# Kernel tuning notes

Hardware: AMD Instinct MI355X
Metric: run time of the kernel (lower is better)

Reference implementation:

```python
import jax, jax.numpy as jnp
import numpy as np

B, S, D = 2, 1024, 1024
N_HEADS = 16
R = 128
M = 8
N_NEURONS = 256


def group_gate(gate, n_basis):
    # gate: [B,S,N] -> [B,S,M], sum over consecutive groups, then normalize
    b, s, n = gate.shape
    gs = n // n_basis  # exact by construction (256/8)
    g = gate.reshape(b, s, n_basis, gs).sum(axis=-1)
    return g / (g.sum(axis=-1, keepdims=True) + 1e-8)


def feature_fn(x, neurons, weights):
    # x:[B,S,D], neurons:[M,D,R], weights:[B,S,M] -> h:[B,S,R]
    all_h = jnp.einsum('bsd,mdr->bsmr', x, neurons)
    return jnp.einsum('bsmr,bsm->bsr', all_h, weights)


def restore_fn(h, neurons, weights):
    # h:[B,S,R], neurons:[M,R,D], weights:[B,S,M] -> [B,S,D]
    pre = jnp.einsum('bsr,bsm->bsmr', h, weights)
    return jnp.einsum('bsmr,mrd->bsd', pre, neurons)


def setup_inputs() -> dict:
    key = jax.random.key(0)
    ks = jax.random.split(key, 9)
    sc = 0.02
    return {
        'x': jax.random.normal(ks[0], (B, S, D), jnp.float32),
        'qk_f': jax.random.normal(ks[1], (M, D, R), jnp.float32) * sc,
        'qk_r': jax.random.normal(ks[2], (M, R, D), jnp.float32) * sc,
        'v_f': jax.random.normal(ks[3], (M, D, R), jnp.float32) * sc,
        'v_r': jax.random.normal(ks[4], (M, R, D), jnp.float32) * sc,
        'Wg_q': jax.random.normal(ks[5], (D, N_NEURONS), jnp.float32) * sc,
        'Wg_k': jax.random.normal(ks[6], (D, N_NEURONS), jnp.float32) * sc,
        'Wg_v': jax.random.normal(ks[7], (D, N_NEURONS), jnp.float32) * sc,
        'W_O': jax.random.normal(ks[8], (D, D), jnp.float32) * sc,
    }


def reference(x, qk_f, qk_r, v_f, v_r, Wg_q, Wg_k, Wg_v, W_O):
    # Router gates (softmax over neuron dim), then grouped per basis
    g_Q = jax.nn.softmax(jnp.einsum('bsd,dn->bsn', x, Wg_q), axis=-1)
    g_K = jax.nn.softmax(jnp.einsum('bsd,dn->bsn', x, Wg_k), axis=-1)
    g_V = jax.nn.softmax(jnp.einsum('bsd,dn->bsn', x, Wg_v), axis=-1)
    gQ_b = group_gate(g_Q, M)
    gK_b = group_gate(g_K, M)
    gV_b = group_gate(g_V, M)

    Q = restore_fn(feature_fn(x, qk_f, gQ_b), qk_r, gQ_b)
    K = restore_fn(feature_fn(x, qk_f, gK_b), qk_r, gK_b)
    V = restore_fn(feature_fn(x, v_f, gV_b), v_r, gV_b)

    d_head = D // N_HEADS
    Q = Q.reshape(B, S, N_HEADS, d_head).transpose(0, 2, 1, 3)
    K = K.reshape(B, S, N_HEADS, d_head).transpose(0, 2, 1, 3)
    V = V.reshape(B, S, N_HEADS, d_head).transpose(0, 2, 1, 3)

    scale = jnp.sqrt(jnp.float32(d_head))
    scores = jnp.einsum('bhsd,bhtd->bhst', Q, K) / scale
    causal = jnp.tril(jnp.ones((S, S), dtype=jnp.bool_))
    scores = jnp.where(causal, scores, jnp.finfo(scores.dtype).min)
    attn_w = jax.nn.softmax(scores, axis=-1)
    out = jnp.einsum('bhst,bhtd->bhsd', attn_w, V)
    out = out.transpose(0, 2, 1, 3).reshape(B, S, D)
    out = jnp.einsum('bsd,de->bse', out, W_O)
    return out
```

## Files before the change

### kernel.cpp

```cpp
#include <hip/hip_runtime.h>
#include <hip/hip_bf16.h>

#define BB 2
#define SS 1024
#define DD 1024
#define NH 16
#define DH 64
#define MM 8
#define RR 128
#define NN 256
#define NT (BB*SS)

using bf16 = __hip_bfloat16;

typedef __attribute__((ext_vector_type(8))) short short8;
typedef __attribute__((ext_vector_type(4))) short short4v;
typedef __attribute__((ext_vector_type(4))) float f32x4;

__device__ __forceinline__ void stf(float* p, size_t i, float v) { p[i] = v; }
__device__ __forceinline__ void stf(bf16* p, size_t i, float v) { p[i] = __float2bfloat16(v); }

#define GLD16(g, l) __builtin_amdgcn_global_load_lds( \
    (const __attribute__((address_space(1))) void*)(g), \
    (__attribute__((address_space(3))) void*)(l), 16, 0, 0)

__device__ __forceinline__ short8 lds_load8(const short* p) {
    short4v a = *(const short4v*)p;
    short4v b = *(const short4v*)(p + 4);
    short8 r;
    r[0] = a[0]; r[1] = a[1]; r[2] = a[2]; r[3] = a[3];
    r[4] = b[0]; r[5] = b[1]; r[6] = b[2]; r[7] = b[3];
    return r;
}

struct GemmZ {
    const bf16* A[5];
    const bf16* Bt[5];
    void* C[5];
    int N[5];
};

template <typename TC, int TAG>
__global__ __launch_bounds__(256) void mfma_gemm_64z(GemmZ P, int Kdim) {
    const int z = blockIdx.z;
    const int Nz = P.N[z];
    const int n0 = blockIdx.x * 128;
    if (n0 >= Nz) return;
    const bf16* __restrict__ A  = P.A[z];
    const bf16* __restrict__ Bt = P.Bt[z];
    TC* __restrict__ C = (TC*)P.C[z];

    const int tid = threadIdx.x;
    const int wave = tid >> 6, lane = tid & 63;
    const int quad = lane >> 4, l15 = lane & 15;
    const int wr = wave >> 1, wc = wave & 1;
    const int m0 = blockIdx.y * 64;

    __shared__ bf16 As[64 * 64];
    __shared__ bf16 Bs[128 * 64];

    f32x4 acc[2][4];
#pragma unroll
    for (int i = 0; i < 2; ++i)
#pragma unroll
        for (int j = 0; j < 4; ++j) acc[i][j] = (f32x4)0.f;

    for (int k0 = 0; k0 < Kdim; k0 += 64) {
        __syncthreads();
#pragma unroll
        for (int i = 0; i < 2; ++i) {
            const int L = i * 256 + wave * 64 + lane;
            const int row = L >> 3;
            const int gch = (L & 7) ^ ((row >> 1) & 7);
            GLD16(A + (size_t)(m0 + row) * Kdim + k0 + gch * 8, &As[(i * 256 + wave * 64) * 8]);
        }
#pragma unroll
        for (int i = 0; i < 4; ++i) {
            const int L = i * 256 + wave * 64 + lane;
            const int row = L >> 3;
            const int gch = (L & 7) ^ ((row >> 1) & 7);
            GLD16(Bt + (size_t)(n0 + row) * Kdim + k0 + gch * 8, &Bs[(i * 256 + wave * 64) * 8]);
        }
        __syncthreads();

#pragma unroll
        for (int kk = 0; kk < 2; ++kk) {
            short8 aF[2], bF[4];
#pragma unroll
            for (int bi = 0; bi < 2; ++bi) {
                int m = wr * 32 + bi * 16 + l15;
                int slot = (kk * 4 + quad) ^ ((m >> 1) & 7);
                aF[bi] = *(const short8*)&As[(m * 8 + slot) * 8];
            }
#pragma unroll
            for (int bj = 0; bj < 4; ++bj) {
                int n = wc * 64 + bj * 16 + l15;
                int slot = (kk * 4 + quad) ^ ((n >> 1) & 7);
                bF[bj] = *(const short8*)&Bs[(n * 8 + slot) * 8];
            }
#pragma unroll
            for (int bi = 0; bi < 2; ++bi)
#pragma unroll
                for (int bj = 0; bj < 4; ++bj)
                    acc[bi][bj] = __builtin_amdgcn_mfma_f32_16x16x32_bf16(aF[bi], bF[bj], acc[bi][bj], 0, 0, 0);
        }
    }

#pragma unroll
    for (int bi = 0; bi < 2; ++bi)
#pragma unroll
        for (int bj = 0; bj < 4; ++bj)
#pragma unroll
            for (int r = 0; r < 4; ++r) {
                int row = m0 + wr * 32 + bi * 16 + quad * 4 + r;
                int col = n0 + wc * 64 + bj * 16 + l15;
                stf(C, (size_t)row * Nz + col, acc[bi][bj][r]);
            }
}

template <typename TC>
__global__ __launch_bounds__(256) void mfma_gemm_64(
    const bf16* __restrict__ A, const bf16* __restrict__ Bt, TC* __restrict__ C,
    int Kdim, int Ndim) {
    const int tid = threadIdx.x;
    const int wave = tid >> 6, lane = tid & 63;
    const int quad = lane >> 4, l15 = lane & 15;
    const int wr = wave >> 1, wc = wave & 1;
    const int m0 = blockIdx.y * 64;
    const int n0 = blockIdx.x * 128;

    __shared__ bf16 As[64 * 64];
    __shared__ bf16 Bs[128 * 64];

    f32x4 acc[2][4];
#pragma unroll
    for (int i = 0; i < 2; ++i)
#pragma unroll
        for (int j = 0; j < 4; ++j) acc[i][j] = (f32x4)0.f;

    for (int k0 = 0; k0 < Kdim; k0 += 64) {
        __syncthreads();
#pragma unroll
        for (int i = 0; i < 2; ++i) {
            const int L = i * 256 + wave * 64 + lane;
            const int row = L >> 3;
            const int gch = (L & 7) ^ ((row >> 1) & 7);
            GLD16(A + (size_t)(m0 + row) * Kdim + k0 + gch * 8, &As[(i * 256 + wave * 64) * 8]);
        }
#pragma unroll
        for (int i = 0; i < 4; ++i) {
            const int L = i * 256 + wave * 64 + lane;
            const int row = L >> 3;
            const int gch = (L & 7) ^ ((row >> 1) & 7);
            GLD16(Bt + (size_t)(n0 + row) * Kdim + k0 + gch * 8, &Bs[(i * 256 + wave * 64) * 8]);
        }
        __syncthreads();

#pragma unroll
        for (int kk = 0; kk < 2; ++kk) {
            short8 aF[2], bF[4];
#pragma unroll
            for (int bi = 0; bi < 2; ++bi) {
                int m = wr * 32 + bi * 16 + l15;
                int slot = (kk * 4 + quad) ^ ((m >> 1) & 7);
                aF[bi] = *(const short8*)&As[(m * 8 + slot) * 8];
            }
#pragma unroll
            for (int bj = 0; bj < 4; ++bj) {
                int n = wc * 64 + bj * 16 + l15;
                int slot = (kk * 4 + quad) ^ ((n >> 1) & 7);
                bF[bj] = *(const short8*)&Bs[(n * 8 + slot) * 8];
            }
#pragma unroll
            for (int bi = 0; bi < 2; ++bi)
#pragma unroll
                for (int bj = 0; bj < 4; ++bj)
                    acc[bi][bj] = __builtin_amdgcn_mfma_f32_16x16x32_bf16(aF[bi], bF[bj], acc[bi][bj], 0, 0, 0);
        }
    }

#pragma unroll
    for (int bi = 0; bi < 2; ++bi)
#pragma unroll
        for (int bj = 0; bj < 4; ++bj)
#pragma unroll
            for (int r = 0; r < 4; ++r) {
                int row = m0 + wr * 32 + bi * 16 + quad * 4 + r;
                int col = n0 + wc * 64 + bj * 16 + l15;
                stf(C, (size_t)row * Ndim + col, acc[bi][bj][r]);
            }
}

struct ConvJobs {
    const float* src[9];
    bf16* dst[9];
    int K[9], R[9], G[9];
    int tEnd[9];
};

__global__ void convert_kernel(ConvJobs J) {
    __shared__ float tile[32][33];
    const int b = blockIdx.x;
    int j = 0;
    while (j < 8 && b >= J.tEnd[j]) ++j;
    const int local = b - (j > 0 ? J.tEnd[j - 1] : 0);
    const float* src = J.src[j];
    bf16* dst = J.dst[j];
    const int tid = threadIdx.x;

    if (J.G[j] == 0) {
        size_t base = (size_t)local * 4096 + (size_t)tid * 16;
        const float4* s4 = (const float4*)(src + base);
        short* d = (short*)(dst + base);
#pragma unroll
        for (int c = 0; c < 4; ++c) {
            float4 v = s4[c];
            short4v o;
            bf16 t0 = __float2bfloat16(v.x); o[0] = *(short*)&t0;
            bf16 t1 = __float2bfloat16(v.y); o[1] = *(short*)&t1;
            bf16 t2 = __float2bfloat16(v.z); o[2] = *(short*)&t2;
            bf16 t3 = __float2bfloat16(v.w); o[3] = *(short*)&t3;
            *(short4v*)(d + c * 4) = o;
        }
    } else {
        const int Kj = J.K[j], Rj = J.R[j];
        const int Rb = Rj >> 5, Kb = Kj >> 5;
        const int perG = Kb * Rb;
        const int g = local / perG;
        const int rem = local - g * perG;
        const int kb = rem / Rb, rb = rem - kb * Rb;
        const int tx = tid & 31, ty0 = tid >> 5;
        const float* s = src + ((size_t)(g * Kj + kb * 32) * Rj) + rb * 32 + tx;
#pragma unroll
        for (int p = 0; p < 4; ++p)
            tile[ty0 + p * 8][tx] = s[(size_t)(ty0 + p * 8) * Rj];
        __syncthreads();
        bf16* dd = dst + ((size_t)(g * Rj + rb * 32) * Kj) + kb * 32 + tx;
#pragma unroll
        for (int p = 0; p < 4; ++p)
            dd[(size_t)(ty0 + p * 8) * Kj] = __float2bfloat16(tile[tx][ty0 + p * 8]);
    }
}

__global__ void gate_combine(const bf16* __restrict__ logitsAll,
                             const bf16* __restrict__ allh,
                             bf16* __restrict__ preQ, bf16* __restrict__ preK,
                             bf16* __restrict__ preV) {
    const int t = blockIdx.x;
    const int n = threadIdx.x;
    const int wave = n >> 6, lane = n & 63;
    __shared__ float wred[3][4];
    __shared__ float sred[3][4];
    __shared__ float gred[3][8];

    float v[3], e[3];
#pragma unroll
    for (int z = 0; z < 3; ++z)
        v[z] = __bfloat162float(logitsAll[(size_t)z * NT * NN + (size_t)t * NN + n]);

    float mz[3];
#pragma unroll
    for (int z = 0; z < 3; ++z) {
        mz[z] = v[z];
#pragma unroll
        for (int off = 1; off <= 32; off <<= 1)
            mz[z] = fmaxf(mz[z], __shfl_xor(mz[z], off));
    }
    if (lane == 0) {
#pragma unroll
        for (int z = 0; z < 3; ++z) wred[z][wave] = mz[z];
    }
    __syncthreads();
    float gmax[3];
#pragma unroll
    for (int z = 0; z < 3; ++z)
        gmax[z] = fmaxf(fmaxf(wred[z][0], wred[z][1]), fmaxf(wred[z][2], wred[z][3]));

    float ws[3];
#pragma unroll
    for (int z = 0; z < 3; ++z) {
        e[z] = __expf(v[z] - gmax[z]);
        ws[z] = e[z];
#pragma unroll
        for (int off = 1; off <= 32; off <<= 1)
            ws[z] += __shfl_xor(ws[z], off);
    }
    if (lane == 0) {
#pragma unroll
        for (int z = 0; z < 3; ++z) sred[z][wave] = ws[z];
    }
    float gs[3];
#pragma unroll
    for (int z = 0; z < 3; ++z) {
        gs[z] = e[z];
#pragma unroll
        for (int off = 1; off <= 16; off <<= 1)
            gs[z] += __shfl_xor(gs[z], off);
    }
    __syncthreads();
    float total[3];
#pragma unroll
    for (int z = 0; z < 3; ++z)
        total[z] = sred[z][0] + sred[z][1] + sred[z][2] + sred[z][3];
    if ((n & 31) == 0) {
#pragma unroll
        for (int z = 0; z < 3; ++z) gred[z][n >> 5] = gs[z] / total[z];
    }
    __syncthreads();

    float gv[3][8];
#pragma unroll
    for (int z = 0; z < 3; ++z) {
        float tot = 0.f;
#pragma unroll
        for (int m = 0; m < 8; ++m) tot += gred[z][m];
        float inv = 1.0f / (tot + 1e-8f);
#pragma unroll
        for (int m = 0; m < 8; ++m) gv[z][m] = gred[z][m] * inv;
    }

    const int r0 = n & 127;
    const int half = n >> 7;
    const bf16* src_qk = allh + (size_t)t * 1024;
    const bf16* src_v  = allh + (size_t)NT * DD + (size_t)t * 1024;
    float hq = 0.f, hk = 0.f, hv = 0.f;
#pragma unroll
    for (int m = 0; m < 8; ++m) {
        float aqk = __bfloat162float(src_qk[m * 128 + r0]);
        float av  = __bfloat162float(src_v[m * 128 + r0]);
        hq += aqk * gv[0][m];
        hk += aqk * gv[1][m];
        hv += av  * gv[2][m];
    }
    __syncthreads();
#pragma unroll
    for (int mm = 0; mm < 4; ++mm) {
        int m = half * 4 + mm;
        size_t o = (size_t)t * 1024 + m * 128 + r0;
        preQ[o] = __float2bfloat16(hq * gv[0][m]);
        preK[o] = __float2bfloat16(hk * gv[1][m]);
        preV[o] = __float2bfloat16(hv * gv[2][m]);
    }
}

#define LDK 68

__global__ __launch_bounds__(256) void flash_attn_split(
    const bf16* __restrict__ Q, const bf16* __restrict__ K,
    const bf16* __restrict__ V, float* __restrict__ Opart,
    float* __restrict__ ml) {
    const int bx = blockIdx.x;
    const int c = bx & 511;
    const int second = bx >> 9;
    const int qt = second ? (c >> 5) : (15 - (c >> 5));
    const int half = second;
    const int bh = c & 31;
    const int b = bh >> 4;
    const int h = bh & 15;
    const int h0 = (qt + 2) >> 1;
    const int kt_lo = half ? h0 : 0;
    const int kt_hi = half ? (qt + 1) : h0;

    const int tid = threadIdx.x;
    const int wave = tid >> 6;
    const int lane = tid & 63;
    const int quad = lane >> 4;
    const int l15 = lane & 15;

    __shared__ short Ks[64 * LDK];
    __shared__ short Vt[64 * LDK];
    __shared__ short Ps[4 * 16 * LDK];

    const int q_row = qt * 64 + wave * 16 + l15;
    const bf16* qptr = Q + (size_t)(b * SS + q_row) * DD + h * DH + quad * 8;
    short8 aq0 = *(const short8*)qptr;
    short8 aq1 = *(const short8*)(qptr + 32);

    float m_r[4], l_r[4];
    f32x4 o[4];
#pragma unroll
    for (int r = 0; r < 4; ++r) { m_r[r] = -3.0e38f; l_r[r] = 0.f; }
#pragma unroll
    for (int cc = 0; cc < 4; ++cc) o[cc] = (f32x4)0.f;

    const float scale = 0.125f;

    for (int kt = kt_lo; kt < kt_hi; ++kt) {
        const int kt0 = kt * 64;
        __syncthreads();
        {
            const int kr = tid >> 2;
            const int dhb = (tid & 3) * 16;
            const bf16* src = K + (size_t)(b * SS + kt0 + kr) * DD + h * DH + dhb;
            short4v v0 = *(const short4v*)(src);
            short4v v1 = *(const short4v*)(src + 4);
            short4v v2 = *(const short4v*)(src + 8);
            short4v v3 = *(const short4v*)(src + 12);
            short* dst = &Ks[kr * LDK + dhb];
            *(short4v*)(dst) = v0;
            *(short4v*)(dst + 4) = v1;
            *(short4v*)(dst + 8) = v2;
            *(short4v*)(dst + 12) = v3;
        }
        {
            const int krp = tid & 31;
            const int dhb = (tid >> 5) * 8;
            const bf16* s0 = V + (size_t)(b * SS + kt0 + 2 * krp) * DD + h * DH + dhb;
            short8 r0 = *(const short8*)s0;
            short8 r1 = *(const short8*)(s0 + DD);
#pragma unroll
            for (int i = 0; i < 8; ++i) {
                unsigned int pk = (unsigned short)r0[i] | ((unsigned int)(unsigned short)r1[i] << 16);
                *(unsigned int*)&Vt[(dhb + i) * LDK + 2 * krp] = pk;
            }
        }
        __syncthreads();

        f32x4 s[4];
#pragma unroll
        for (int cc = 0; cc < 4; ++cc) {
            short8 bk0 = lds_load8(&Ks[(cc * 16 + l15) * LDK + quad * 8]);
            short8 bk1 = lds_load8(&Ks[(cc * 16 + l15) * LDK + 32 + quad * 8]);
            f32x4 acc = (f32x4)0.f;
            acc = __builtin_amdgcn_mfma_f32_16x16x32_bf16(aq0, bk0, acc, 0, 0, 0);
            acc = __builtin_amdgcn_mfma_f32_16x16x32_bf16(aq1, bk1, acc, 0, 0, 0);
            s[cc] = acc;
        }

        const bool diag = (kt == qt);
#pragma unroll
        for (int cc = 0; cc < 4; ++cc) {
#pragma unroll
            for (int r = 0; r < 4; ++r) {
                float v = s[cc][r] * scale;
                if (diag) {
                    int row_rel = wave * 16 + quad * 4 + r;
                    int col_rel = cc * 16 + l15;
                    if (col_rel > row_rel) v = -3.0e38f;
                }
                s[cc][r] = v;
            }
        }

        float p[4][4];
        float alpha[4];
#pragma unroll
        for (int r = 0; r < 4; ++r) {
            float mx = fmaxf(fmaxf(s[0][r], s[1][r]), fmaxf(s[2][r], s[3][r]));
            mx = fmaxf(mx, __shfl_xor(mx, 1));
            mx = fmaxf(mx, __shfl_xor(mx, 2));
            mx = fmaxf(mx, __shfl_xor(mx, 4));
            mx = fmaxf(mx, __shfl_xor(mx, 8));
            float new_m = fmaxf(m_r[r], mx);
            alpha[r] = __expf(m_r[r] - new_m);
            float rs = 0.f;
#pragma unroll
            for (int cc = 0; cc < 4; ++cc) {
                float e = __expf(s[cc][r] - new_m);
                p[cc][r] = e;
                rs += e;
            }
            rs += __shfl_xor(rs, 1);
            rs += __shfl_xor(rs, 2);
            rs += __shfl_xor(rs, 4);
            rs += __shfl_xor(rs, 8);
            l_r[r] = l_r[r] * alpha[r] + rs;
            m_r[r] = new_m;
        }
#pragma unroll
        for (int cc = 0; cc < 4; ++cc)
#pragma unroll
            for (int r = 0; r < 4; ++r) o[cc][r] *= alpha[r];

        short* pw = &Ps[wave * 16 * LDK];
#pragma unroll
        for (int cc = 0; cc < 4; ++cc)
#pragma unroll
            for (int r = 0; r < 4; ++r) {
                bf16 hb = __float2bfloat16(p[cc][r]);
                pw[(quad * 4 + r) * LDK + cc * 16 + l15] = *(short*)&hb;
            }

        short8 ap0 = lds_load8(&pw[l15 * LDK + quad * 8]);
        short8 ap1 = lds_load8(&pw[l15 * LDK + 32 + quad * 8]);

#pragma unroll
        for (int cc = 0; cc < 4; ++cc) {
            short8 bv0 = lds_load8(&Vt[(cc * 16 + l15) * LDK + quad * 8]);
            short8 bv1 = lds_load8(&Vt[(cc * 16 + l15) * LDK + 32 + quad * 8]);
            o[cc] = __builtin_amdgcn_mfma_f32_16x16x32_bf16(ap0, bv0, o[cc], 0, 0, 0);
            o[cc] = __builtin_amdgcn_mfma_f32_16x16x32_bf16(ap1, bv1, o[cc], 0, 0, 0);
        }
    }

    const int idx = (half * 32 + bh) * 16 + qt;
    float* ob = Opart + (size_t)idx * 4096;
#pragma unroll
    for (int cc = 0; cc < 4; ++cc)
#pragma unroll
        for (int r = 0; r < 4; ++r) {
            int row = wave * 16 + quad * 4 + r;
            ob[row * 64 + cc * 16 + l15] = o[cc][r];
        }
    if (l15 == 0) {
#pragma unroll
        for (int r = 0; r < 4; ++r) {
            int row = wave * 16 + quad * 4 + r;
            ml[(size_t)idx * 128 + row] = m_r[r];
            ml[(size_t)idx * 128 + 64 + row] = l_r[r];
        }
    }
}

__global__ void attn_combine(const float* __restrict__ Opart,
                             const float* __restrict__ ml,
                             bf16* __restrict__ out) {
    const int bidx = blockIdx.x;
    const int bh = bidx >> 4;
    const int qt = bidx & 15;
    const int b = bh >> 4;
    const int h = bh & 15;
    const int tid = threadIdx.x;
    const int row = tid >> 2;
    const int cg = tid & 3;

    const int p0 = bh * 16 + qt;
    const int p1 = 512 + bh * 16 + qt;
    float m0 = ml[(size_t)p0 * 128 + row], l0 = ml[(size_t)p0 * 128 + 64 + row];
    float m1 = ml[(size_t)p1 * 128 + row], l1 = ml[(size_t)p1 * 128 + 64 + row];
    float ms = fmaxf(m0, m1);
    float w0 = __expf(m0 - ms), w1 = __expf(m1 - ms);
    float inv = 1.0f / (l0 * w0 + l1 * w1);

    const float* o0 = Opart + (size_t)p0 * 4096 + row * 64 + cg * 16;
    const float* o1 = Opart + (size_t)p1 * 4096 + row * 64 + cg * 16;
    short out16[16];
#pragma unroll
    for (int j = 0; j < 16; j += 4) {
        float4 a = *(const float4*)(o0 + j);
        float4 bb = *(const float4*)(o1 + j);
        float v0 = (a.x * w0 + bb.x * w1) * inv;
        float v1 = (a.y * w0 + bb.y * w1) * inv;
        float v2 = (a.z * w0 + bb.z * w1) * inv;
        float v3 = (a.w * w0 + bb.w * w1) * inv;
        bf16 t0 = __float2bfloat16(v0); out16[j] = *(short*)&t0;
        bf16 t1 = __float2bfloat16(v1); out16[j + 1] = *(short*)&t1;
        bf16 t2 = __float2bfloat16(v2); out16[j + 2] = *(short*)&t2;
        bf16 t3 = __float2bfloat16(v3); out16[j + 3] = *(short*)&t3;
    }
    short* dst = (short*)(out + (size_t)(b * SS + qt * 64 + row) * DD + h * DH + cg * 16);
    *(short8*)dst = *(short8*)&out16[0];
    *(short8*)(dst + 8) = *(short8*)&out16[8];
}

extern "C" void kernel_launch(void* const* d_in, const int* in_sizes, int n_in,
                              void* d_out, int out_size, void* d_ws, size_t ws_size,
                              hipStream_t stream) {
    const float* x    = (const float*)d_in[0];
    const float* qk_f = (const float*)d_in[1];
    const float* qk_r = (const float*)d_in[2];
    const float* v_f  = (const float*)d_in[3];
    const float* v_r  = (const float*)d_in[4];
    const float* Wg_q = (const float*)d_in[5];
    const float* Wg_k = (const float*)d_in[6];
    const float* Wg_v = (const float*)d_in[7];
    const float* W_O  = (const float*)d_in[8];

    char* w = (char*)d_ws;
    const size_t MB = 1 << 20;
    bf16* xb     = (bf16*)(w + 0);
    bf16* wg_bt  = (bf16*)(w + 4 * MB);
    bf16* fbt    = (bf16*)(w + (size_t)(5.5 * MB));
    bf16* logits = (bf16*)(w + (size_t)(9.5 * MB));
    bf16* qkr_bt = (bf16*)(w + 16 * MB);
    bf16* vr_bt  = (bf16*)(w + 18 * MB);
    bf16* wo_bt  = (bf16*)(w + 20 * MB);
    bf16* preQ   = (bf16*)(w + 0);
    bf16* preK   = (bf16*)(w + 4 * MB);
    bf16* Kb     = (bf16*)(w + 8 * MB);
    bf16* Vb     = (bf16*)(w + 12 * MB);
    bf16* attnb  = (bf16*)(w + 0);
    float* Opart = (float*)(w + 32 * MB);
    float* mlbuf = (float*)(w + 48 * MB);
    bf16* allh   = (bf16*)d_out;
    bf16* preV   = allh + (size_t)NT * DD;
    bf16* Qb     = (bf16*)d_out;
    float* out   = (float*)d_out;

    ConvJobs J;
    J.src[0] = qk_f; J.dst[0] = fbt;              J.K[0] = 1024; J.R[0] = 128;  J.G[0] = 8;
    J.src[1] = v_f;  J.dst[1] = fbt + 1024*1024;  J.K[1] = 1024; J.R[1] = 128;  J.G[1] = 8;
    J.src[2] = qk_r; J.dst[2] = qkr_bt;           J.K[2] = 1024; J.R[2] = 1024; J.G[2] = 1;
    J.src[3] = v_r;  J.dst[3] = vr_bt;            J.K[3] = 1024; J.R[3] = 1024; J.G[3] = 1;
    J.src[4] = W_O;  J.dst[4] = wo_bt;            J.K[4] = 1024; J.R[4] = 1024; J.G[4] = 1;
    J.src[5] = Wg_q; J.dst[5] = wg_bt;            J.K[5] = 1024; J.R[5] = 256;  J.G[5] = 1;
    J.src[6] = Wg_k; J.dst[6] = wg_bt + 256*1024; J.K[6] = 1024; J.R[6] = 256;  J.G[6] = 1;
    J.src[7] = Wg_v; J.dst[7] = wg_bt + 2*256*1024; J.K[7] = 1024; J.R[7] = 256; J.G[7] = 1;
    J.src[8] = x;    J.dst[8] = xb;               J.K[8] = 0;    J.R[8] = 0;    J.G[8] = 0;
    int tiles[9] = {1024, 1024, 1024, 1024, 1024, 256, 256, 256, 512};
    int cum = 0;
    for (int i = 0; i < 9; ++i) { cum += tiles[i]; J.tEnd[i] = cum; }
    convert_kernel<<<cum, 256, 0, stream>>>(J);

    GemmZ Pp;
    Pp.A[0] = Pp.A[1] = Pp.A[2] = Pp.A[3] = Pp.A[4] = xb;
    Pp.Bt[0] = fbt;             Pp.Bt[1] = fbt + 1024*1024;
    Pp.Bt[2] = wg_bt;           Pp.Bt[3] = wg_bt + 256*1024;  Pp.Bt[4] = wg_bt + 2*256*1024;
    Pp.C[0] = allh;             Pp.C[1] = allh + (size_t)NT * DD;
    Pp.C[2] = logits;           Pp.C[3] = logits + (size_t)NT * NN;
    Pp.C[4] = logits + 2 * (size_t)NT * NN;
    Pp.N[0] = 1024; Pp.N[1] = 1024; Pp.N[2] = 256; Pp.N[3] = 256; Pp.N[4] = 256;
    mfma_gemm_64z<bf16, 0><<<dim3(8, 32, 5), 256, 0, stream>>>(Pp, DD);

    gate_combine<<<NT, 256, 0, stream>>>(logits, allh, preQ, preK, preV);

    GemmZ Pr;
    Pr.A[0] = preQ; Pr.A[1] = preK; Pr.A[2] = preV;
    Pr.Bt[0] = qkr_bt; Pr.Bt[1] = qkr_bt; Pr.Bt[2] = vr_bt;
    Pr.C[0] = Qb; Pr.C[1] = Kb; Pr.C[2] = Vb;
    Pr.N[0] = Pr.N[1] = Pr.N[2] = 1024;
    Pr.A[3] = Pr.A[4] = nullptr; Pr.Bt[3] = Pr.Bt[4] = nullptr;
    Pr.C[3] = Pr.C[4] = nullptr; Pr.N[3] = Pr.N[4] = 0;
    mfma_gemm_64z<bf16, 1><<<dim3(8, 32, 3), 256, 0, stream>>>(Pr, DD);

    flash_attn_split<<<dim3(1024), 256, 0, stream>>>(Qb, Kb, Vb, Opart, mlbuf);

    attn_combine<<<dim3(512), 256, 0, stream>>>(Opart, mlbuf, attnb);

    mfma_gemm_64<float><<<dim3(8, 32), 256, 0, stream>>>(attnb, wo_bt, out, DD, DD);
}
```

Measured before the change: 205.9 us.

## Double-buffer K/V tiles in flash attention and compact projection GEMM grid

Flash attention now double-buffers its K and V tiles in LDS. The next K tile is issued via global_load_lds into a swizzled layout, and the next V tile is loaded into registers, while the current tile is being computed. This hides global load latency and removes one barrier per iteration, at the cost of more LDS. The projection GEMM launch is flattened to 704 blocks, so early-exit blocks for the narrower 256-wide gate GEMMs are no longer launched. GEMM kernels are also refactored to share one device body function.

```diff
diff --git a/kernel.cpp b/kernel.cpp
--- a/kernel.cpp
+++ b/kernel.cpp
@@ -33,6 +33,74 @@
     return r;
 }
 
+template <typename TC>
+__device__ __forceinline__ void gemm64_body(
+    const bf16* __restrict__ A, const bf16* __restrict__ Bt, TC* __restrict__ C,
+    int Kdim, int Nz, int m0, int n0, bf16* As, bf16* Bs) {
+    const int tid = threadIdx.x;
+    const int wave = tid >> 6, lane = tid & 63;
+    const int quad = lane >> 4, l15 = lane & 15;
+    const int wr = wave >> 1, wc = wave & 1;
+
+    f32x4 acc[2][4];
+#pragma unroll
+    for (int i = 0; i < 2; ++i)
+#pragma unroll
+        for (int j = 0; j < 4; ++j) acc[i][j] = (f32x4)0.f;
+
+    for (int k0 = 0; k0 < Kdim; k0 += 64) {
+        __syncthreads();
+#pragma unroll
+        for (int i = 0; i < 2; ++i) {
+            const int L = i * 256 + wave * 64 + lane;
+            const int row = L >> 3;
+            const int gch = (L & 7) ^ ((row >> 1) & 7);
+            GLD16(A + (size_t)(m0 + row) * Kdim + k0 + gch * 8, &As[(i * 256 + wave * 64) * 8]);
+        }
+#pragma unroll
+        for (int i = 0; i < 4; ++i) {
+            const int L = i * 256 + wave * 64 + lane;
+            const int row = L >> 3;
+            const int gch = (L & 7) ^ ((row >> 1) & 7);
+            GLD16(Bt + (size_t)(n0 + row) * Kdim + k0 + gch * 8, &Bs[(i * 256 + wave * 64) * 8]);
+        }
+        __syncthreads();
+
+#pragma unroll
+        for (int kk = 0; kk < 2; ++kk) {
+            short8 aF[2], bF[4];
+#pragma unroll
+            for (int bi = 0; bi < 2; ++bi) {
+                int m = wr * 32 + bi * 16 + l15;
+                int slot = (kk * 4 + quad) ^ ((m >> 1) & 7);
+                aF[bi] = *(const short8*)&As[(m * 8 + slot) * 8];
+            }
+#pragma unroll
+            for (int bj = 0; bj < 4; ++bj) {
+                int n = wc * 64 + bj * 16 + l15;
+                int slot = (kk * 4 + quad) ^ ((n >> 1) & 7);
+                bF[bj] = *(const short8*)&Bs[(n * 8 + slot) * 8];
+            }
+#pragma unroll
+            for (int bi = 0; bi < 2; ++bi)
+#pragma unroll
+                for (int bj = 0; bj < 4; ++bj)
+                    acc[bi][bj] = __builtin_amdgcn_mfma_f32_16x16x32_bf16(aF[bi], bF[bj], acc[bi][bj], 0, 0, 0);
+        }
+    }
+
+#pragma unroll
+    for (int bi = 0; bi < 2; ++bi)
+#pragma unroll
+        for (int bj = 0; bj < 4; ++bj)
+#pragma unroll
+            for (int r = 0; r < 4; ++r) {
+                int row = m0 + wr * 32 + bi * 16 + quad * 4 + r;
+                int col = n0 + wc * 64 + bj * 16 + l15;
+                stf(C, (size_t)row * Nz + col, acc[bi][bj][r]);
+            }
+}
+
 struct GemmZ {
     const bf16* A[5];
     const bf16* Bt[5];
@@ -40,155 +108,30 @@
     int N[5];
 };
 
-template <typename TC, int TAG>
-__global__ __launch_bounds__(256) void mfma_gemm_64z(GemmZ P, int Kdim) {
-    const int z = blockIdx.z;
-    const int Nz = P.N[z];
-    const int n0 = blockIdx.x * 128;
-    if (n0 >= Nz) return;
-    const bf16* __restrict__ A  = P.A[z];
-    const bf16* __restrict__ Bt = P.Bt[z];
-    TC* __restrict__ C = (TC*)P.C[z];
-
-    const int tid = threadIdx.x;
-    const int wave = tid >> 6, lane = tid & 63;
-    const int quad = lane >> 4, l15 = lane & 15;
-    const int wr = wave >> 1, wc = wave & 1;
-    const int m0 = blockIdx.y * 64;
-
+__global__ __launch_bounds__(256) void mfma_proj(GemmZ P, int Kdim) {
     __shared__ bf16 As[64 * 64];
     __shared__ bf16 Bs[128 * 64];
-
-    f32x4 acc[2][4];
-#pragma unroll
-    for (int i = 0; i < 2; ++i)
-#pragma unroll
-        for (int j = 0; j < 4; ++j) acc[i][j] = (f32x4)0.f;
-
-    for (int k0 = 0; k0 < Kdim; k0 += 64) {
-        __syncthreads();
-#pragma unroll
-        for (int i = 0; i < 2; ++i) {
-            const int L = i * 256 + wave * 64 + lane;
-            const int row = L >> 3;
-            const int gch = (L & 7) ^ ((row >> 1) & 7);
-            GLD16(A + (size_t)(m0 + row) * Kdim + k0 + gch * 8, &As[(i * 256 + wave * 64) * 8]);
-        }
-#pragma unroll
-        for (int i = 0; i < 4; ++i) {
-            const int L = i * 256 + wave * 64 + lane;
-            const int row = L >> 3;
-            const int gch = (L & 7) ^ ((row >> 1) & 7);
-            GLD16(Bt + (size_t)(n0 + row) * Kdim + k0 + gch * 8, &Bs[(i * 256 + wave * 64) * 8]);
-        }
-        __syncthreads();
-
-#pragma unroll
-        for (int kk = 0; kk < 2; ++kk) {
-            short8 aF[2], bF[4];
-#pragma unroll
-            for (int bi = 0; bi < 2; ++bi) {
-                int m = wr * 32 + bi * 16 + l15;
-                int slot = (kk * 4 + quad) ^ ((m >> 1) & 7);
-                aF[bi] = *(const short8*)&As[(m * 8 + slot) * 8];
-            }
-#pragma unroll
-            for (int bj = 0; bj < 4; ++bj) {
-                int n = wc * 64 + bj * 16 + l15;
-                int slot = (kk * 4 + quad) ^ ((n >> 1) & 7);
-                bF[bj] = *(const short8*)&Bs[(n * 8 + slot) * 8];
-            }
-#pragma unroll
-            for (int bi = 0; bi < 2; ++bi)
-#pragma unroll
-                for (int bj = 0; bj < 4; ++bj)
-                    acc[bi][bj] = __builtin_amdgcn_mfma_f32_16x16x32_bf16(aF[bi], bF[bj], acc[bi][bj], 0, 0, 0);
-        }
-    }
-
-#pragma unroll
-    for (int bi = 0; bi < 2; ++bi)
-#pragma unroll
-        for (int bj = 0; bj < 4; ++bj)
-#pragma unroll
-            for (int r = 0; r < 4; ++r) {
-                int row = m0 + wr * 32 + bi * 16 + quad * 4 + r;
-                int col = n0 + wc * 64 + bj * 16 + l15;
-                stf(C, (size_t)row * Nz + col, acc[bi][bj][r]);
-            }
-}
-
-template <typename TC>
-__global__ __launch_bounds__(256) void mfma_gemm_64(
-    const bf16* __restrict__ A, const bf16* __restrict__ Bt, TC* __restrict__ C,
-    int Kdim, int Ndim) {
-    const int tid = threadIdx.x;
-    const int wave = tid >> 6, lane = tid & 63;
-    const int quad = lane >> 4, l15 = lane & 15;
-    const int wr = wave >> 1, wc = wave & 1;
-    const int m0 = blockIdx.y * 64;
-    const int n0 = blockIdx.x * 128;
-
+    const int bidx = blockIdx.x;
+    int z, xx, yy;
+    if (bidx < 512) { z = bidx >> 8; int r = bidx & 255; yy = r >> 3; xx = r & 7; }
+    else { int r = bidx - 512; z = 2 + r / 64; r = r % 64; yy = r >> 1; xx = r & 1; }
+    gemm64_body<bf16>(P.A[z], P.Bt[z], (bf16*)P.C[z], Kdim, P.N[z], yy * 64, xx * 128, As, Bs);
+}
+
+__global__ __launch_bounds__(256) void mfma_restore(GemmZ P, int Kdim) {
     __shared__ bf16 As[64 * 64];
     __shared__ bf16 Bs[128 * 64];
-
-    f32x4 acc[2][4];
-#pragma unroll
-    for (int i = 0; i < 2; ++i)
-#pragma unroll
-        for (int j = 0; j < 4; ++j) acc[i][j] = (f32x4)0.f;
-
-    for (int k0 = 0; k0 < Kdim; k0 += 64) {
-        __syncthreads();
-#pragma unroll
-        for (int i = 0; i < 2; ++i) {
-            const int L = i * 256 + wave * 64 + lane;
-            const int row = L >> 3;
-            const int gch = (L & 7) ^ ((row >> 1) & 7);
-            GLD16(A + (size_t)(m0 + row) * Kdim + k0 + gch * 8, &As[(i * 256 + wave * 64) * 8]);
-        }
-#pragma unroll
-        for (int i = 0; i < 4; ++i) {
-            const int L = i * 256 + wave * 64 + lane;
-            const int row = L >> 3;
-            const int gch = (L & 7) ^ ((row >> 1) & 7);
-            GLD16(Bt + (size_t)(n0 + row) * Kdim + k0 + gch * 8, &Bs[(i * 256 + wave * 64) * 8]);
-        }
-        __syncthreads();
-
-#pragma unroll
-        for (int kk = 0; kk < 2; ++kk) {
-            short8 aF[2], bF[4];
-#pragma unroll
-            for (int bi = 0; bi < 2; ++bi) {
-                int m = wr * 32 + bi * 16 + l15;
-                int slot = (kk * 4 + quad) ^ ((m >> 1) & 7);
-                aF[bi] = *(const short8*)&As[(m * 8 + slot) * 8];
-            }
-#pragma unroll
-            for (int bj = 0; bj < 4; ++bj) {
-                int n = wc * 64 + bj * 16 + l15;
-                int slot = (kk * 4 + quad) ^ ((n >> 1) & 7);
-                bF[bj] = *(const short8*)&Bs[(n * 8 + slot) * 8];
-            }
-#pragma unroll
-            for (int bi = 0; bi < 2; ++bi)
-#pragma unroll
-                for (int bj = 0; bj < 4; ++bj)
-                    acc[bi][bj] = __builtin_amdgcn_mfma_f32_16x16x32_bf16(aF[bi], bF[bj], acc[bi][bj], 0, 0, 0);
-        }
-    }
-
-#pragma unroll
-    for (int bi = 0; bi < 2; ++bi)
-#pragma unroll
-        for (int bj = 0; bj < 4; ++bj)
-#pragma unroll
-            for (int r = 0; r < 4; ++r) {
-                int row = m0 + wr * 32 + bi * 16 + quad * 4 + r;
-                int col = n0 + wc * 64 + bj * 16 + l15;
-                stf(C, (size_t)row * Ndim + col, acc[bi][bj][r]);
-            }
+    const int z = blockIdx.z;
+    gemm64_body<bf16>(P.A[z], P.Bt[z], (bf16*)P.C[z], Kdim, P.N[z],
+                      blockIdx.y * 64, blockIdx.x * 128, As, Bs);
+}
+
+__global__ __launch_bounds__(256) void mfma_gemm_64(
+    const bf16* __restrict__ A, const bf16* __restrict__ Bt, float* __restrict__ C,
+    int Kdim, int Ndim) {
+    __shared__ bf16 As[64 * 64];
+    __shared__ bf16 Bs[128 * 64];
+    gemm64_body<float>(A, Bt, C, Kdim, Ndim, blockIdx.y * 64, blockIdx.x * 128, As, Bs);
 }
 
 struct ConvJobs {
@@ -367,8 +310,8 @@
     const int quad = lane >> 4;
     const int l15 = lane & 15;
 
-    __shared__ short Ks[64 * LDK];
-    __shared__ short Vt[64 * LDK];
+    __shared__ short Ks[2][64 * 64];
+    __shared__ short Vt[2][64 * LDK];
     __shared__ short Ps[4 * 16 * LDK];
 
     const int q_row = qt * 64 + wave * 16 + l15;
@@ -376,6 +319,9 @@
     short8 aq0 = *(const short8*)qptr;
     short8 aq1 = *(const short8*)(qptr + 32);
 
+    const int krp = tid & 31;
+    const int dhb = (tid >> 5) * 8;
+
     float m_r[4], l_r[4];
     f32x4 o[4];
 #pragma unroll
@@ -385,42 +331,53 @@
 
     const float scale = 0.125f;
 
+    if (kt_lo < kt_hi) {
+#pragma unroll
+        for (int i = 0; i < 2; ++i) {
+            const int L = i * 256 + wave * 64 + lane;
+            const int row = L >> 3;
+            const int gch = (L & 7) ^ ((row >> 1) & 7);
+            GLD16(K + (size_t)(b * SS + kt_lo * 64 + row) * DD + h * DH + gch * 8,
+                  &Ks[0][(i * 256 + wave * 64) * 8]);
+        }
+        const bf16* s0 = V + (size_t)(b * SS + kt_lo * 64 + 2 * krp) * DD + h * DH + dhb;
+        short8 r0 = *(const short8*)s0;
+        short8 r1 = *(const short8*)(s0 + DD);
+#pragma unroll
+        for (int i = 0; i < 8; ++i) {
+            unsigned int pk = (unsigned short)r0[i] | ((unsigned int)(unsigned short)r1[i] << 16);
+            *(unsigned int*)&Vt[0][(dhb + i) * LDK + 2 * krp] = pk;
+        }
+        __syncthreads();
+    }
+
     for (int kt = kt_lo; kt < kt_hi; ++kt) {
-        const int kt0 = kt * 64;
-        __syncthreads();
-        {
-            const int kr = tid >> 2;
-            const int dhb = (tid & 3) * 16;
-            const bf16* src = K + (size_t)(b * SS + kt0 + kr) * DD + h * DH + dhb;
-            short4v v0 = *(const short4v*)(src);
-            short4v v1 = *(const short4v*)(src + 4);
-            short4v v2 = *(const short4v*)(src + 8);
-            short4v v3 = *(const short4v*)(src + 12);
-            short* dst = &Ks[kr * LDK + dhb];
-            *(short4v*)(dst) = v0;
-            *(short4v*)(dst + 4) = v1;
-            *(short4v*)(dst + 8) = v2;
-            *(short4v*)(dst + 12) = v3;
-        }
-        {
-            const int krp = tid & 31;
-            const int dhb = (tid >> 5) * 8;
-            const bf16* s0 = V + (size_t)(b * SS + kt0 + 2 * krp) * DD + h * DH + dhb;
-            short8 r0 = *(const short8*)s0;
-            short8 r1 = *(const short8*)(s0 + DD);
-#pragma unroll
-            for (int i = 0; i < 8; ++i) {
-                unsigned int pk = (unsigned short)r0[i] | ((unsigned int)(unsigned short)r1[i] << 16);
-                *(unsigned int*)&Vt[(dhb + i) * LDK + 2 * krp] = pk;
-            }
-        }
-        __syncthreads();
-
+        const int buf = (kt - kt_lo) & 1;
+        const bool pf = (kt + 1 < kt_hi);
+        short8 pr0, pr1;
+        if (pf) {
+#pragma unroll
+            for (int i = 0; i < 2; ++i) {
+                const int L = i * 256 + wave * 64 + lane;
+                const int row = L >> 3;
+                const int gch = (L & 7) ^ ((row >> 1) & 7);
+                GLD16(K + (size_t)(b * SS + (kt + 1) * 64 + row) * DD + h * DH + gch * 8,
+                      &Ks[buf ^ 1][(i * 256 + wave * 64) * 8]);
+            }
+            const bf16* s0 = V + (size_t)(b * SS + (kt + 1) * 64 + 2 * krp) * DD + h * DH + dhb;
+            pr0 = *(const short8*)s0;
+            pr1 = *(const short8*)(s0 + DD);
+        }
+
+        const short* KsB = Ks[buf];
         f32x4 s[4];
 #pragma unroll
         for (int cc = 0; cc < 4; ++cc) {
-            short8 bk0 = lds_load8(&Ks[(cc * 16 + l15) * LDK + quad * 8]);
-            short8 bk1 = lds_load8(&Ks[(cc * 16 + l15) * LDK + 32 + quad * 8]);
+            int n = cc * 16 + l15;
+            int sl0 = quad ^ ((n >> 1) & 7);
+            int sl1 = (quad + 4) ^ ((n >> 1) & 7);
+            short8 bk0 = *(const short8*)&KsB[(n * 8 + sl0) * 8];
+            short8 bk1 = *(const short8*)&KsB[(n * 8 + sl1) * 8];
             f32x4 acc = (f32x4)0.f;
             acc = __builtin_amdgcn_mfma_f32_16x16x32_bf16(aq0, bk0, acc, 0, 0, 0);
             acc = __builtin_amdgcn_mfma_f32_16x16x32_bf16(aq1, bk1, acc, 0, 0, 0);
@@ -484,13 +441,23 @@
         short8 ap0 = lds_load8(&pw[l15 * LDK + quad * 8]);
         short8 ap1 = lds_load8(&pw[l15 * LDK + 32 + quad * 8]);
 
+        const short* VtB = Vt[buf];
 #pragma unroll
         for (int cc = 0; cc < 4; ++cc) {
-            short8 bv0 = lds_load8(&Vt[(cc * 16 + l15) * LDK + quad * 8]);
-            short8 bv1 = lds_load8(&Vt[(cc * 16 + l15) * LDK + 32 + quad * 8]);
+            short8 bv0 = lds_load8(&VtB[(cc * 16 + l15) * LDK + quad * 8]);
+            short8 bv1 = lds_load8(&VtB[(cc * 16 + l15) * LDK + 32 + quad * 8]);
             o[cc] = __builtin_amdgcn_mfma_f32_16x16x32_bf16(ap0, bv0, o[cc], 0, 0, 0);
             o[cc] = __builtin_amdgcn_mfma_f32_16x16x32_bf16(ap1, bv1, o[cc], 0, 0, 0);
         }
+
+        if (pf) {
+#pragma unroll
+            for (int i = 0; i < 8; ++i) {
+                unsigned int pk = (unsigned short)pr0[i] | ((unsigned int)(unsigned short)pr1[i] << 16);
+                *(unsigned int*)&Vt[buf ^ 1][(dhb + i) * LDK + 2 * krp] = pk;
+            }
+        }
+        __syncthreads();
     }
 
     const int idx = (half * 32 + bh) * 16 + qt;
@@ -610,7 +577,7 @@
     Pp.C[2] = logits;           Pp.C[3] = logits + (size_t)NT * NN;
     Pp.C[4] = logits + 2 * (size_t)NT * NN;
     Pp.N[0] = 1024; Pp.N[1] = 1024; Pp.N[2] = 256; Pp.N[3] = 256; Pp.N[4] = 256;
-    mfma_gemm_64z<bf16, 0><<<dim3(8, 32, 5), 256, 0, stream>>>(Pp, DD);
+    mfma_proj<<<dim3(704), 256, 0, stream>>>(Pp, DD);
 
     gate_combine<<<NT, 256, 0, stream>>>(logits, allh, preQ, preK, preV);
 
@@ -621,11 +588,11 @@
     Pr.N[0] = Pr.N[1] = Pr.N[2] = 1024;
     Pr.A[3] = Pr.A[4] = nullptr; Pr.Bt[3] = Pr.Bt[4] = nullptr;
     Pr.C[3] = Pr.C[4] = nullptr; Pr.N[3] = Pr.N[4] = 0;
-    mfma_gemm_64z<bf16, 1><<<dim3(8, 32, 3), 256, 0, stream>>>(Pr, DD);
+    mfma_restore<<<dim3(8, 32, 3), 256, 0, stream>>>(Pr, DD);
 
     flash_attn_split<<<dim3(1024), 256, 0, stream>>>(Qb, Kb, Vb, Opart, mlbuf);
 
     attn_combine<<<dim3(512), 256, 0, stream>>>(Opart, mlbuf, attnb);
 
-    mfma_gemm_64<float><<<dim3(8, 32), 256, 0, stream>>>(attnb, wo_bt, out, DD, DD);
-}
+    mfma_gemm_64<<<dim3(8, 32), 256, 0, stream>>>(attnb, wo_bt, out, DD, DD);
+}
```

New measurement: 195.9 us. 4.8% less time.
